# Performance work log

Hardware: AMD Instinct MI355X
Metric: run time of the kernel (lower is better)

The kernel has to match this reference:

```python
import jax, jax.numpy as jnp
import numpy as np

# ---- skeleton topology constants (match init_kwargs) ----
E = 28          # unpooled edges
P = 14          # pooled regions
C = 16          # channels per edge
K = 3           # conv kernel size
ADJ = [sorted(set([max(i - 1, 0), i, min(i + 1, E - 1)])) for i in range(E)]
POOLED = [[2 * r, 2 * r + 1] for r in range(P)]

# unpool scatter map: edge e <- region UNPOOL_IDX[e]
UNPOOL_IDX = np.zeros(E, dtype=np.int32)
for r, region in enumerate(POOLED):
    for e in region:
        UNPOOL_IDX[e] = r

# adjacency mask for the skeletal conv weight [E*C, E*C, K]
_MASK = np.zeros((E * C, E * C, 1), dtype=np.float32)
for eo in range(E):
    for ei in ADJ[eo]:
        _MASK[eo * C:(eo + 1) * C, ei * C:(ei + 1) * C, :] = 1.0
MASK = jnp.asarray(_MASK)


def upsample_linear_2x(x):
    """torch nn.Upsample(scale_factor=2, mode='linear', align_corners=False) on [B,C,T]."""
    T = x.shape[-1]
    pos = (jnp.arange(2 * T, dtype=x.dtype) + 0.5) / 2.0 - 0.5
    i0 = jnp.floor(pos)
    w1 = (pos - i0)[None, None, :]
    i0 = i0.astype(jnp.int32)
    lo = jnp.clip(i0, 0, T - 1)
    hi = jnp.clip(i0 + 1, 0, T - 1)
    return x[..., lo] * (1.0 - w1) + x[..., hi] * w1


def setup_inputs() -> dict:
    key = jax.random.key(0)
    k1, k2, k3 = jax.random.split(key, 3)
    x = jax.random.normal(k1, (16, P * C, 4096), dtype=jnp.float32)
    weight = jax.random.normal(k2, (E * C, E * C, K), dtype=jnp.float32) * 0.02
    bias = jax.random.normal(k3, (E * C,), dtype=jnp.float32) * 0.02
    return {"x": x, "weight": weight, "bias": bias}


def reference(x, weight, bias):
    y = upsample_linear_2x(x)
    B, _, T2 = y.shape
    # UnPool: scatter each pooled region's channels to all its member edges
    y = y.reshape(B, P, C, T2)[:, jnp.asarray(UNPOOL_IDX)].reshape(B, E * C, T2)
    # SkeletalConv: adjacency-masked conv1d, stride 1, padding 1
    w = weight * MASK.astype(weight.dtype)
    out = jax.lax.conv_general_dilated(
        y, w, window_strides=(1,), padding=[(1, 1)],
        dimension_numbers=("NCH", "OIH", "NCH"))
    out = out + bias[None, :, None]
    # LeakyReLU(0.2)
    return jnp.where(out >= 0, out, 0.2 * out)
```

## Files before the change

### kernel.cpp

```cpp
#include <hip/hip_runtime.h>

typedef __bf16 bf16x8_t __attribute__((ext_vector_type(8)));
typedef float  f32x4_t  __attribute__((ext_vector_type(4)));
typedef float  f32x2_t  __attribute__((ext_vector_type(2)));
typedef int    i32x4_t  __attribute__((ext_vector_type(4)));

#define EDGES 28
#define TIN   4096
#define T2V   8192
#define NB    16
#define CIN   224
#define COUT  448

__device__ __forceinline__ unsigned short f2bf(float f) {
    unsigned int u = __builtin_bit_cast(unsigned int, f);
    u = (u + 0x7fffu + ((u >> 16) & 1u)) >> 16;
    return (unsigned short)u;
}
__device__ __forceinline__ float bf2f(unsigned short h) {
    unsigned int u = ((unsigned int)h) << 16;
    return __builtin_bit_cast(float, u);
}

__device__ __forceinline__ int lds_byte(int mr, int ch) {
    return (mr << 7) + ((((ch >> 3) ^ (mr & 7))) << 4) + ((ch & 7) << 1);
}

__global__ __launch_bounds__(256)
void prep_fold(const float* __restrict__ w,
               unsigned short* __restrict__ abf,
               float* __restrict__ wc0,
               float* __restrict__ wc2) {
    int tid = blockIdx.x * 256 + threadIdx.x;
    int e = tid & 7;
    int l = (tid >> 3) & 63;
    int rest = tid >> 9;
    int d = rest % 3;
    int sd = rest / 3;
    int s = sd & 1;
    int eo = sd >> 1;
    int co = l & 15;
    int j = (l >> 4) * 8 + e;
    int slot = j >> 4, ci = j & 15;
    int r0 = (eo == 0) ? 0 : ((eo - 1) >> 1);
    int r1 = (eo == EDGES - 1) ? ((EDGES - 1) >> 1) : ((eo + 1) >> 1);
    int elo = (eo == 0) ? 0 : eo - 1;
    int ehi = (eo == EDGES - 1) ? EDGES - 1 : eo + 1;
    float W0 = 0.f, W1 = 0.f, W2 = 0.f;
    for (int ei = elo; ei <= ehi; ++ei) {
        int re = ei >> 1;
        bool take = slot ? (r1 != r0 && re == r1) : (re == r0);
        if (!take) continue;
        const float* wp = w + ((size_t)(eo * 16 + co) * COUT + (ei * 16 + ci)) * 3;
        W0 += wp[0]; W1 += wp[1]; W2 += wp[2];
    }
    float a;
    if (s == 0) {
        a = (d == 0) ? 0.75f * W0 + 0.25f * W1
          : (d == 1) ? 0.25f * W0 + 0.75f * W1 + 0.75f * W2
                     : 0.25f * W2;
    } else {
        a = (d == 0) ? 0.25f * W0
          : (d == 1) ? 0.75f * W0 + 0.75f * W1 + 0.25f * W2
                     : 0.25f * W1 + 0.75f * W2;
    }
    abf[tid] = f2bf(a);
    if (s == 0 && d == 0) {
        wc0[(eo * 16 + co) * 32 + j] = W0;
        wc2[(eo * 16 + co) * 32 + j] = W2;
    }
}

__global__ __launch_bounds__(256, 4)
void skel_main(const float* __restrict__ x,
               const float* __restrict__ bias,
               const unsigned short* __restrict__ abf,
               const float* __restrict__ wc0,
               const float* __restrict__ wc2,
               float* __restrict__ out) {
    __shared__ __align__(16) unsigned short lds[258 * 64];
    const int tb = blockIdx.x;
    const int r  = blockIdx.y;
    const int b  = blockIdx.z;
    const int t  = threadIdx.x;
    const int mstart = tb << 8;
    const int reg0 = (r == 0) ? 0 : r - 1;
    const int reg2 = (r == 13) ? 13 : r + 1;

    #pragma unroll
    for (int pass = 0; pass < 2; ++pass) {
        int task = t + pass * 256;
        if (task < 384) {
            int g  = task >> 6;
            int mq = task & 63;
            int rgb = g >> 1;
            int reg = (rgb == 0) ? reg0 : ((rgb == 1) ? r : reg2);
            const float* xb = x + ((size_t)b * CIN + reg * 16 + (g & 1) * 8) * TIN
                              + mstart + 4 * mq;
            f32x4_t vf[8];
            #pragma unroll
            for (int i = 0; i < 8; ++i)
                vf[i] = *(const f32x4_t*)(xb + (size_t)i * TIN);
            #pragma unroll
            for (int q = 0; q < 4; ++q) {
                int qq = (q + mq) & 3;
                int mr = 1 + 4 * mq + qq;
                i32x4_t u;
                #pragma unroll
                for (int j = 0; j < 4; ++j)
                    u[j] = (int)((unsigned int)f2bf(vf[2 * j][qq]) |
                                 ((unsigned int)f2bf(vf[2 * j + 1][qq]) << 16));
                int byte = (mr << 7) + (((g ^ (mr & 7))) << 4);
                *(i32x4_t*)((char*)lds + byte) = u;
            }
        }
    }
    if (t < 96) {
        int ch = (t < 48) ? t : t - 48;
        int rg = ch >> 4;
        int reg = (rg == 0) ? reg0 : ((rg == 1) ? r : reg2);
        int gch = reg * 16 + (ch & 15);
        int mr, m;
        if (t < 48) { mr = 0;   m = mstart - 1;   if (m < 0) m = 0; }
        else        { mr = 257; m = mstart + 256; if (m > TIN - 1) m = TIN - 1; }
        float v = x[((size_t)b * CIN + gch) * TIN + m];
        *(unsigned short*)((char*)lds + lds_byte(mr, ch)) = f2bf(v);
    }

    const int l  = t & 63;
    const int wv = t >> 6;
    const int lc = l & 15;
    const int lg = l >> 4;

    __syncthreads();

    #pragma unroll
    for (int ei = 0; ei < 2; ++ei) {
        const int eo = 2 * r + ei;
        const int chb = 16 * ei;
        bf16x8_t afr[2][3];
        #pragma unroll
        for (int s = 0; s < 2; ++s)
            #pragma unroll
            for (int d = 0; d < 3; ++d) {
                int4 tmp = *(const int4*)(abf + (size_t)(((eo * 2 + s) * 3 + d) * 64 + l) * 8);
                afr[s][d] = __builtin_bit_cast(bf16x8_t, tmp);
            }
        float bco[4];
        #pragma unroll
        for (int rr = 0; rr < 4; ++rr) bco[rr] = bias[eo * 16 + lg * 4 + rr];
        float* ob = out + ((size_t)b * COUT + eo * 16) * (size_t)T2V;

        #pragma unroll
        for (int tile = 0; tile < 4; ++tile) {
            int mloc = wv * 64 + tile * 16;
            f32x4_t acc0 = {0.f, 0.f, 0.f, 0.f};
            f32x4_t acc1 = {0.f, 0.f, 0.f, 0.f};
            #pragma unroll
            for (int d = 0; d < 3; ++d) {
                int lmr = mloc + lc + d;
                int4 bd = *(const int4*)((char*)lds + lds_byte(lmr, chb + 8 * lg));
                bf16x8_t bfr = __builtin_bit_cast(bf16x8_t, bd);
                acc0 = __builtin_amdgcn_mfma_f32_16x16x32_bf16(afr[0][d], bfr, acc0, 0, 0, 0);
                acc1 = __builtin_amdgcn_mfma_f32_16x16x32_bf16(afr[1][d], bfr, acc1, 0, 0, 0);
            }
            int mcol = mstart + mloc + lc;
            if (tb == 0 && mloc == 0 && lc == 0) {
                #pragma unroll
                for (int rr = 0; rr < 4; ++rr) {
                    int co = lg * 4 + rr; float sum = 0.f;
                    for (int j = 0; j < 32; ++j)
                        sum += wc0[(eo * 16 + co) * 32 + j] *
                               bf2f(*(const unsigned short*)((char*)lds + lds_byte(1, chb + j)));
                    acc0[rr] -= sum;
                }
            }
            if (tb == (TIN / 256 - 1) && mloc == 240 && lc == 15) {
                #pragma unroll
                for (int rr = 0; rr < 4; ++rr) {
                    int co = lg * 4 + rr; float sum = 0.f;
                    for (int j = 0; j < 32; ++j)
                        sum += wc2[(eo * 16 + co) * 32 + j] *
                               bf2f(*(const unsigned short*)((char*)lds + lds_byte(256, chb + j)));
                    acc1[rr] -= sum;
                }
            }
            #pragma unroll
            for (int rr = 0; rr < 4; ++rr) {
                int co = lg * 4 + rr;
                float e = acc0[rr] + bco[rr];
                float o = acc1[rr] + bco[rr];
                e = (e >= 0.f) ? e : 0.2f * e;
                o = (o >= 0.f) ? o : 0.2f * o;
                f32x2_t pk = {e, o};
                __builtin_nontemporal_store(pk, (f32x2_t*)(ob + (size_t)co * T2V + 2 * mcol));
            }
        }
    }
}

extern "C" void kernel_launch(void* const* d_in, const int* in_sizes, int n_in,
                              void* d_out, int out_size, void* d_ws, size_t ws_size,
                              hipStream_t stream) {
    const float* x    = (const float*)d_in[0];
    const float* w    = (const float*)d_in[1];
    const float* bias = (const float*)d_in[2];
    float* out = (float*)d_out;

    unsigned short* abf = (unsigned short*)d_ws;
    float* wc0 = (float*)((char*)d_ws + 172032);
    float* wc2 = (float*)((char*)d_ws + 172032 + 57344);

    prep_fold<<<336, 256, 0, stream>>>(w, abf, wc0, wc2);
    dim3 grid(TIN / 256, 14, NB);
    skel_main<<<grid, 256, 0, stream>>>(x, bias, abf, wc0, wc2, out);
}
```

Baseline: 89.72 us.

## Process two time tiles per block with software-pipelined prefetch of next tile

Each block now handles two consecutive 256-step time tiles instead of one, halving the grid. The global loads for the second tile are issued before the first tile's MFMA compute and stores, so load latency can overlap with compute. In exchange, the kernel needs more registers for the prefetched data, adds extra barriers, and launches half as many blocks, which lowers parallelism.

```diff
diff --git a/kernel.cpp b/kernel.cpp
--- a/kernel.cpp
+++ b/kernel.cpp
@@ -79,124 +79,163 @@
                const float* __restrict__ wc2,
                float* __restrict__ out) {
     __shared__ __align__(16) unsigned short lds[258 * 64];
-    const int tb = blockIdx.x;
+    const int sq = blockIdx.x;
     const int r  = blockIdx.y;
     const int b  = blockIdx.z;
     const int t  = threadIdx.x;
-    const int mstart = tb << 8;
     const int reg0 = (r == 0) ? 0 : r - 1;
     const int reg2 = (r == 13) ? 13 : r + 1;
-
-    #pragma unroll
-    for (int pass = 0; pass < 2; ++pass) {
-        int task = t + pass * 256;
-        if (task < 384) {
-            int g  = task >> 6;
-            int mq = task & 63;
-            int rgb = g >> 1;
-            int reg = (rgb == 0) ? reg0 : ((rgb == 1) ? r : reg2);
-            const float* xb = x + ((size_t)b * CIN + reg * 16 + (g & 1) * 8) * TIN
-                              + mstart + 4 * mq;
-            f32x4_t vf[8];
-            #pragma unroll
-            for (int i = 0; i < 8; ++i)
-                vf[i] = *(const f32x4_t*)(xb + (size_t)i * TIN);
-            #pragma unroll
-            for (int q = 0; q < 4; ++q) {
-                int qq = (q + mq) & 3;
-                int mr = 1 + 4 * mq + qq;
-                i32x4_t u;
-                #pragma unroll
-                for (int j = 0; j < 4; ++j)
-                    u[j] = (int)((unsigned int)f2bf(vf[2 * j][qq]) |
-                                 ((unsigned int)f2bf(vf[2 * j + 1][qq]) << 16));
-                int byte = (mr << 7) + (((g ^ (mr & 7))) << 4);
-                *(i32x4_t*)((char*)lds + byte) = u;
-            }
-        }
-    }
-    if (t < 96) {
-        int ch = (t < 48) ? t : t - 48;
-        int rg = ch >> 4;
-        int reg = (rg == 0) ? reg0 : ((rg == 1) ? r : reg2);
-        int gch = reg * 16 + (ch & 15);
-        int mr, m;
-        if (t < 48) { mr = 0;   m = mstart - 1;   if (m < 0) m = 0; }
-        else        { mr = 257; m = mstart + 256; if (m > TIN - 1) m = TIN - 1; }
-        float v = x[((size_t)b * CIN + gch) * TIN + m];
-        *(unsigned short*)((char*)lds + lds_byte(mr, ch)) = f2bf(v);
-    }
 
     const int l  = t & 63;
     const int wv = t >> 6;
     const int lc = l & 15;
     const int lg = l >> 4;
 
-    __syncthreads();
-
-    #pragma unroll
-    for (int ei = 0; ei < 2; ++ei) {
-        const int eo = 2 * r + ei;
-        const int chb = 16 * ei;
-        bf16x8_t afr[2][3];
-        #pragma unroll
-        for (int s = 0; s < 2; ++s)
-            #pragma unroll
-            for (int d = 0; d < 3; ++d) {
-                int4 tmp = *(const int4*)(abf + (size_t)(((eo * 2 + s) * 3 + d) * 64 + l) * 8);
-                afr[s][d] = __builtin_bit_cast(bf16x8_t, tmp);
-            }
-        float bco[4];
-        #pragma unroll
-        for (int rr = 0; rr < 4; ++rr) bco[rr] = bias[eo * 16 + lg * 4 + rr];
-        float* ob = out + ((size_t)b * COUT + eo * 16) * (size_t)T2V;
-
-        #pragma unroll
-        for (int tile = 0; tile < 4; ++tile) {
-            int mloc = wv * 64 + tile * 16;
-            f32x4_t acc0 = {0.f, 0.f, 0.f, 0.f};
-            f32x4_t acc1 = {0.f, 0.f, 0.f, 0.f};
-            #pragma unroll
-            for (int d = 0; d < 3; ++d) {
-                int lmr = mloc + lc + d;
-                int4 bd = *(const int4*)((char*)lds + lds_byte(lmr, chb + 8 * lg));
-                bf16x8_t bfr = __builtin_bit_cast(bf16x8_t, bd);
-                acc0 = __builtin_amdgcn_mfma_f32_16x16x32_bf16(afr[0][d], bfr, acc0, 0, 0, 0);
-                acc1 = __builtin_amdgcn_mfma_f32_16x16x32_bf16(afr[1][d], bfr, acc1, 0, 0, 0);
-            }
-            int mcol = mstart + mloc + lc;
-            if (tb == 0 && mloc == 0 && lc == 0) {
+    const int gA = t >> 6, mqA = t & 63;
+    const int rgbA = gA >> 1;
+    const int regA = (rgbA == 0) ? reg0 : ((rgbA == 1) ? r : reg2);
+    const int gB = 4 + (t >> 6);
+    const int mqB = t & 63;
+    const int hch = (t < 48) ? t : t - 48;
+    const int hrg = hch >> 4;
+    const int hreg = (hrg == 0) ? reg0 : ((hrg == 1) ? r : reg2);
+    const int hgch = hreg * 16 + (hch & 15);
+
+    const float* xbA = x + ((size_t)b * CIN + regA * 16 + (gA & 1) * 8) * TIN + 4 * mqA;
+    const float* xbB = x + ((size_t)b * CIN + reg2 * 16 + (gB & 1) * 8) * TIN + 4 * mqB;
+
+    const int mst0 = sq * 512;
+    const int mst1 = mst0 + 256;
+
+    auto stage_write = [&](const f32x4_t (&vf)[8], int g, int mq) {
+        #pragma unroll
+        for (int p = 0; p < 4; ++p) {
+            int qv = (p + mq) & 3;
+            int mr = 1 + 4 * mq + qv;
+            i32x4_t u;
+            #pragma unroll
+            for (int j = 0; j < 4; ++j)
+                u[j] = (int)((unsigned int)f2bf(vf[2 * j][qv]) |
+                             ((unsigned int)f2bf(vf[2 * j + 1][qv]) << 16));
+            int byte = (mr << 7) + (((g ^ (mr & 7))) << 4);
+            *(i32x4_t*)((char*)lds + byte) = u;
+        }
+    };
+
+    auto compute_store = [&](int mstart, int tb) {
+        #pragma unroll
+        for (int ei = 0; ei < 2; ++ei) {
+            const int eo = 2 * r + ei;
+            const int chb = 16 * ei;
+            bf16x8_t afr[2][3];
+            #pragma unroll
+            for (int s = 0; s < 2; ++s)
+                #pragma unroll
+                for (int d = 0; d < 3; ++d) {
+                    int4 tmp = *(const int4*)(abf + (size_t)(((eo * 2 + s) * 3 + d) * 64 + l) * 8);
+                    afr[s][d] = __builtin_bit_cast(bf16x8_t, tmp);
+                }
+            float bco[4];
+            #pragma unroll
+            for (int rr = 0; rr < 4; ++rr) bco[rr] = bias[eo * 16 + lg * 4 + rr];
+            float* ob = out + ((size_t)b * COUT + eo * 16) * (size_t)T2V;
+
+            #pragma unroll
+            for (int tl = 0; tl < 4; ++tl) {
+                int mloc = wv * 64 + tl * 16;
+                f32x4_t acc0 = {0.f, 0.f, 0.f, 0.f};
+                f32x4_t acc1 = {0.f, 0.f, 0.f, 0.f};
+                #pragma unroll
+                for (int d = 0; d < 3; ++d) {
+                    int lmr = mloc + lc + d;
+                    int4 bd = *(const int4*)((char*)lds + lds_byte(lmr, chb + 8 * lg));
+                    bf16x8_t bfr = __builtin_bit_cast(bf16x8_t, bd);
+                    acc0 = __builtin_amdgcn_mfma_f32_16x16x32_bf16(afr[0][d], bfr, acc0, 0, 0, 0);
+                    acc1 = __builtin_amdgcn_mfma_f32_16x16x32_bf16(afr[1][d], bfr, acc1, 0, 0, 0);
+                }
+                int mcol = mstart + mloc + lc;
+                if (tb == 0 && mloc == 0 && lc == 0) {
+                    #pragma unroll
+                    for (int rr = 0; rr < 4; ++rr) {
+                        int co = lg * 4 + rr; float sum = 0.f;
+                        for (int j = 0; j < 32; ++j)
+                            sum += wc0[(eo * 16 + co) * 32 + j] *
+                                   bf2f(*(const unsigned short*)((char*)lds + lds_byte(1, chb + j)));
+                        acc0[rr] -= sum;
+                    }
+                }
+                if (tb == (TIN / 256 - 1) && mloc == 240 && lc == 15) {
+                    #pragma unroll
+                    for (int rr = 0; rr < 4; ++rr) {
+                        int co = lg * 4 + rr; float sum = 0.f;
+                        for (int j = 0; j < 32; ++j)
+                            sum += wc2[(eo * 16 + co) * 32 + j] *
+                                   bf2f(*(const unsigned short*)((char*)lds + lds_byte(256, chb + j)));
+                        acc1[rr] -= sum;
+                    }
+                }
                 #pragma unroll
                 for (int rr = 0; rr < 4; ++rr) {
-                    int co = lg * 4 + rr; float sum = 0.f;
-                    for (int j = 0; j < 32; ++j)
-                        sum += wc0[(eo * 16 + co) * 32 + j] *
-                               bf2f(*(const unsigned short*)((char*)lds + lds_byte(1, chb + j)));
-                    acc0[rr] -= sum;
-                }
-            }
-            if (tb == (TIN / 256 - 1) && mloc == 240 && lc == 15) {
-                #pragma unroll
-                for (int rr = 0; rr < 4; ++rr) {
-                    int co = lg * 4 + rr; float sum = 0.f;
-                    for (int j = 0; j < 32; ++j)
-                        sum += wc2[(eo * 16 + co) * 32 + j] *
-                               bf2f(*(const unsigned short*)((char*)lds + lds_byte(256, chb + j)));
-                    acc1[rr] -= sum;
-                }
-            }
-            #pragma unroll
-            for (int rr = 0; rr < 4; ++rr) {
-                int co = lg * 4 + rr;
-                float e = acc0[rr] + bco[rr];
-                float o = acc1[rr] + bco[rr];
-                e = (e >= 0.f) ? e : 0.2f * e;
-                o = (o >= 0.f) ? o : 0.2f * o;
-                f32x2_t pk = {e, o};
-                __builtin_nontemporal_store(pk, (f32x2_t*)(ob + (size_t)co * T2V + 2 * mcol));
+                    int co = lg * 4 + rr;
+                    float e = acc0[rr] + bco[rr];
+                    float o = acc1[rr] + bco[rr];
+                    e = (e >= 0.f) ? e : 0.2f * e;
+                    o = (o >= 0.f) ? o : 0.2f * o;
+                    f32x2_t pk = {e, o};
+                    __builtin_nontemporal_store(pk, (f32x2_t*)(ob + (size_t)co * T2V + 2 * mcol));
+                }
             }
         }
-    }
+    };
+
+    f32x4_t vp[8], vs[8], vp2[8];
+    float hv, hv2;
+
+    #pragma unroll
+    for (int i = 0; i < 8; ++i) vp[i] = *(const f32x4_t*)(xbA + (size_t)i * TIN + mst0);
+    if (t < 128) {
+        #pragma unroll
+        for (int i = 0; i < 8; ++i) vs[i] = *(const f32x4_t*)(xbB + (size_t)i * TIN + mst0);
+    }
+    if (t < 96) {
+        int m = (t < 48) ? mst0 - 1 : mst0 + 256;
+        if (m < 0) m = 0;
+        hv = x[((size_t)b * CIN + hgch) * TIN + m];
+    }
+
+    stage_write(vp, gA, mqA);
+    if (t < 128) stage_write(vs, gB, mqB);
+    if (t < 96) {
+        int mr = (t < 48) ? 0 : 257;
+        *(unsigned short*)((char*)lds + lds_byte(mr, hch)) = f2bf(hv);
+    }
+    __syncthreads();
+
+    #pragma unroll
+    for (int i = 0; i < 8; ++i) vp2[i] = *(const f32x4_t*)(xbA + (size_t)i * TIN + mst1);
+    if (t < 96) {
+        int m = (t < 48) ? mst1 - 1 : mst1 + 256;
+        if (m > TIN - 1) m = TIN - 1;
+        hv2 = x[((size_t)b * CIN + hgch) * TIN + m];
+    }
+
+    compute_store(mst0, 2 * sq);
+
+    if (t < 128) {
+        #pragma unroll
+        for (int i = 0; i < 8; ++i) vs[i] = *(const f32x4_t*)(xbB + (size_t)i * TIN + mst1);
+    }
+    __syncthreads();
+
+    stage_write(vp2, gA, mqA);
+    if (t < 128) stage_write(vs, gB, mqB);
+    if (t < 96) {
+        int mr = (t < 48) ? 0 : 257;
+        *(unsigned short*)((char*)lds + lds_byte(mr, hch)) = f2bf(hv2);
+    }
+    __syncthreads();
+
+    compute_store(mst1, 2 * sq + 1);
 }
 
 extern "C" void kernel_launch(void* const* d_in, const int* in_sizes, int n_in,
@@ -212,6 +251,6 @@
     float* wc2 = (float*)((char*)d_ws + 172032 + 57344);
 
     prep_fold<<<336, 256, 0, stream>>>(w, abf, wc0, wc2);
-    dim3 grid(TIN / 256, 14, NB);
+    dim3 grid(TIN / 512, 14, NB);
     skel_main<<<grid, 256, 0, stream>>>(x, bias, abf, wc0, wc2, out);
 }
```

Result: slower. 229.5 us (+155.8%).
